# Kernel optimization log

Hardware: AMD Instinct MI355X
Metric: run time of the kernel (lower is better)

## Reference

```python
import jax, jax.numpy as jnp
import numpy as np

LN_EPS = 1e-5

def _ln(x, g, b):
    m = x.mean(-1, keepdims=True)
    v = ((x - m) ** 2).mean(-1, keepdims=True)
    return (x - m) / jnp.sqrt(v + LN_EPS) * g + b

def _mlp(x, W1, b1, g, beta, W2, b2):
    # Linear -> LayerNorm -> ReLU -> Linear
    h = jax.nn.relu(_ln(x @ W1 + b1, g, beta))
    return h @ W2 + b2

def setup_inputs() -> dict:
    key = jax.random.key(0)
    N, E, C_in, C_out, H = 50000, 800000, 64, 64, 64
    ks = jax.random.split(key, 16)
    def rn(k, shape, fan_in):
        return jax.random.normal(k, shape, jnp.float32) * (fan_in ** -0.5)
    return dict(
        x=jax.random.normal(ks[0], (N, C_in), jnp.float32),
        pos=jax.random.normal(ks[1], (N, 3), jnp.float32),
        edge_index=jax.random.randint(ks[2], (2, E), 0, N, jnp.int32),
        W_in=rn(ks[3], (C_in, C_in), C_in), b_in=jnp.zeros((C_in,), jnp.float32),
        W_lin=rn(ks[4], (C_in, C_out), C_in),
        W_src=rn(ks[5], (C_in, C_out), C_in),
        W_dst=rn(ks[6], (C_in, C_out), C_in),
        pos_W1=rn(ks[7], (3, H), 3), pos_b1=jnp.zeros((H,), jnp.float32),
        pos_g=jnp.ones((H,), jnp.float32), pos_beta=jnp.zeros((H,), jnp.float32),
        pos_W2=rn(ks[8], (H, C_out), H), pos_b2=jnp.zeros((C_out,), jnp.float32),
        att_W1=rn(ks[9], (C_out, H), C_out), att_b1=jnp.zeros((H,), jnp.float32),
        att_g=jnp.ones((H,), jnp.float32), att_beta=jnp.zeros((H,), jnp.float32),
        att_W2=rn(ks[10], (H, C_out), H), att_b2=jnp.zeros((C_out,), jnp.float32),
        W_out=rn(ks[11], (C_out, C_out), C_out), b_out=jnp.zeros((C_out,), jnp.float32),
    )

def reference(x, pos, edge_index, W_in, b_in, W_lin, W_src, W_dst,
              pos_W1, pos_b1, pos_g, pos_beta, pos_W2, pos_b2,
              att_W1, att_b1, att_g, att_beta, att_W2, att_b2,
              W_out, b_out):
    N = x.shape[0]
    # lin_in + relu
    x = jax.nn.relu(x @ W_in + b_in)
    # PointTransformerConv with add_self_loops=True (PyG default)
    loops = jnp.arange(N, dtype=edge_index.dtype)
    src = jnp.concatenate([edge_index[0], loops])  # j (neighbors)
    dst = jnp.concatenate([edge_index[1], loops])  # i (centers)
    a_src = x @ W_src           # [N, C_out]
    a_dst = x @ W_dst           # [N, C_out]
    v = x @ W_lin               # [N, C_out]
    # per-edge positional encoding delta = pos_nn(pos_i - pos_j)
    delta = _mlp(pos[dst] - pos[src], pos_W1, pos_b1, pos_g, pos_beta, pos_W2, pos_b2)  # [E, C_out]
    alpha = _mlp(a_dst[dst] - a_src[src] + delta, att_W1, att_b1, att_g, att_beta, att_W2, att_b2)
    # per-destination, per-channel softmax over variable-size neighborhoods
    amax = jax.ops.segment_max(alpha, dst, num_segments=N)
    e = jnp.exp(alpha - amax[dst])
    denom = jax.ops.segment_sum(e, dst, num_segments=N)
    w = e / jnp.clip(denom[dst], 1e-16)
    # weighted scatter-sum of (value_j + delta)
    out = jax.ops.segment_sum(w * (v[src] + delta), dst, num_segments=N)  # [N, C_out]
    # lin_out + relu
    return jax.nn.relu(out @ W_out + b_out)
```

## Files before the change

### kernel.cpp

```cpp
#include <hip/hip_runtime.h>
#include <hip/hip_bf16.h>


typedef __bf16 bf16x8 __attribute__((ext_vector_type(8)));
typedef short  s16x8  __attribute__((ext_vector_type(8)));
typedef float  f32x4  __attribute__((ext_vector_type(4)));

#define SWZ(b) ((b) ^ ((((b) >> 7) & 7) << 4))
#define MAXSEG 16

__device__ __forceinline__ unsigned short f2b(float f) {
  union { __hip_bfloat16 h; unsigned short u; } c;
  c.h = __float2bfloat16(f);
  return c.u;
}
__device__ __forceinline__ unsigned int pack2(float a, float b) {
  return (unsigned int)f2b(a) | ((unsigned int)f2b(b) << 16);
}

__device__ __forceinline__ void stage_wt(const float* __restrict__ W, char* dst, int tid) {
  for (int idx = tid; idx < 2048; idx += 256) {
    int c  = idx >> 5;
    int k2 = (idx & 31) << 1;
    float v0 = W[k2 * 64 + c];
    float v1 = W[(k2 + 1) * 64 + c];
    int byte = c * 128 + k2 * 2;
    *(unsigned int*)(dst + SWZ(byte)) = pack2(v0, v1);
  }
}

__device__ __forceinline__ void gemm64(const char* actb, const char* wb,
                                       int ew, int g, int m, f32x4 acc[4]) {
  #pragma unroll
  for (int kk = 0; kk < 2; kk++) {
    s16x8 af = *(const s16x8*)(actb + SWZ((ew + m) * 128 + g * 16 + kk * 64));
    #pragma unroll
    for (int t = 0; t < 4; t++) {
      s16x8 bf = *(const s16x8*)(wb + SWZ((t * 16 + m) * 128 + g * 16 + kk * 64));
      acc[t] = __builtin_amdgcn_mfma_f32_16x16x32_bf16(
          __builtin_bit_cast(bf16x8, af), __builtin_bit_cast(bf16x8, bf), acc[t], 0, 0, 0);
    }
  }
}

__global__ __launch_bounds__(256, 3) void node_mfma_kernel(
    const float* __restrict__ x,
    const float* __restrict__ W_in, const float* __restrict__ b_in,
    const float* __restrict__ W_lin, const float* __restrict__ W_src, const float* __restrict__ W_dst,
    float* __restrict__ a_src, float* __restrict__ a_dst, float* __restrict__ vv,
    int N)
{
  __shared__ __align__(16) char sWinT[8192], sWsT[8192], sWdT[8192], sWlT[8192], sX[8192];
  __shared__ float sB[64];
  int tid = threadIdx.x;
  stage_wt(W_in,  sWinT, tid);
  stage_wt(W_src, sWsT,  tid);
  stage_wt(W_dst, sWdT,  tid);
  stage_wt(W_lin, sWlT,  tid);
  if (tid < 64) sB[tid] = b_in[tid];

  const int lane = tid & 63, wv = tid >> 6;
  const int g = lane >> 4, m = lane & 15;
  const int ew = wv << 4;
  const int srow = tid >> 2, sc0 = (tid & 3) << 4;
  const int ntile = (N + 63) >> 6;

  for (int tile = blockIdx.x; tile < ntile; tile += gridDim.x) {
    const int rbase = tile << 6;
    __syncthreads();
    {
      int gr = rbase + srow; if (gr >= N) gr = N - 1;
      const float4* src = (const float4*)&x[(size_t)gr * 64 + sc0];
      #pragma unroll
      for (int q = 0; q < 4; q++) {
        float4 f = src[q];
        int byte = srow * 128 + sc0 * 2 + q * 8;
        *(unsigned int*)(sX + SWZ(byte))     = pack2(f.x, f.y);
        *(unsigned int*)(sX + SWZ(byte + 4)) = pack2(f.z, f.w);
      }
    }
    __syncthreads();

    f32x4 a0[4] = {};
    gemm64(sX, sWinT, ew, g, m, a0);
    float x1[4][4];
    #pragma unroll
    for (int t = 0; t < 4; t++)
      #pragma unroll
      for (int r = 0; r < 4; r++) x1[t][r] = fmaxf(a0[t][r] + sB[t * 16 + m], 0.f);
    __syncthreads();
    #pragma unroll
    for (int t = 0; t < 4; t++)
      #pragma unroll
      for (int r = 0; r < 4; r++)
        *(unsigned short*)(sX + SWZ((ew + 4 * g + r) * 128 + (t * 16 + m) * 2)) = f2b(x1[t][r]);
    __syncthreads();

    f32x4 as[4] = {}, ad[4] = {}, al[4] = {};
    gemm64(sX, sWsT, ew, g, m, as);
    gemm64(sX, sWdT, ew, g, m, ad);
    gemm64(sX, sWlT, ew, g, m, al);
    #pragma unroll
    for (int t = 0; t < 4; t++)
      #pragma unroll
      for (int r = 0; r < 4; r++) {
        int gr = rbase + ew + 4 * g + r;
        if (gr < N) {
          size_t o = (size_t)gr * 64 + t * 16 + m;
          a_src[o] = as[t][r]; a_dst[o] = ad[t][r]; vv[o] = al[t][r];
        }
      }
  }
}

__global__ void hist_kernel(const int* __restrict__ ei, int* __restrict__ deg, int E, int Etot) {
  int stride = gridDim.x * blockDim.x;
  for (int e = blockIdx.x * blockDim.x + threadIdx.x; e < Etot; e += stride) {
    int d = (e < E) ? ei[E + e] : (e - E);
    atomicAdd(&deg[d], 1);
  }
}

__global__ __launch_bounds__(256) void scanA_kernel(const int* __restrict__ deg, int* __restrict__ chunkSum, int N) {
  __shared__ int s[256];
  int i = blockIdx.x * 256 + threadIdx.x;
  s[threadIdx.x] = (i < N) ? deg[i] : 0;
  __syncthreads();
  for (int off = 128; off > 0; off >>= 1) {
    if (threadIdx.x < off) s[threadIdx.x] += s[threadIdx.x + off];
    __syncthreads();
  }
  if (threadIdx.x == 0) chunkSum[blockIdx.x] = s[0];
}

__global__ __launch_bounds__(256) void scanB_kernel(const int* __restrict__ chunkSum, int* __restrict__ chunkPre, int nchunk) {
  __shared__ int s[256];
  int t = threadIdx.x;
  int v = (t < nchunk) ? chunkSum[t] : 0;
  s[t] = v; __syncthreads();
  for (int off = 1; off < 256; off <<= 1) {
    int x = (t >= off) ? s[t - off] : 0;
    __syncthreads();
    s[t] += x;
    __syncthreads();
  }
  if (t < nchunk) chunkPre[t] = s[t] - v;
}

__global__ __launch_bounds__(256) void scanC_kernel(const int* __restrict__ deg, const int* __restrict__ chunkPre,
                                                    int* __restrict__ cursor, int N) {
  __shared__ int s[256];
  int t = threadIdx.x;
  int i = blockIdx.x * 256 + t;
  int v = (i < N) ? deg[i] : 0;
  s[t] = v; __syncthreads();
  for (int off = 1; off < 256; off <<= 1) {
    int x = (t >= off) ? s[t - off] : 0;
    __syncthreads();
    s[t] += x;
    __syncthreads();
  }
  if (i < N) cursor[i] = chunkPre[blockIdx.x] + s[t] - v;
}

__global__ void scatter_kernel(const int* __restrict__ ei, int* __restrict__ cursor, int* __restrict__ perm,
                               int E, int Etot) {
  int stride = gridDim.x * blockDim.x;
  for (int e = blockIdx.x * blockDim.x + threadIdx.x; e < Etot; e += stride) {
    int d = (e < E) ? ei[E + e] : (e - E);
    int p = atomicAdd(&cursor[d], 1);
    perm[p] = e;
  }
}

__global__ __launch_bounds__(256, 3) void edge_kernel(
    const float* __restrict__ pos, const int* __restrict__ ei, const int* __restrict__ perm,
    const float* __restrict__ a_src_g, const float* __restrict__ a_dst_g, const float* __restrict__ v_g,
    const float* __restrict__ pos_W1, const float* __restrict__ pos_b1,
    const float* __restrict__ pos_gg, const float* __restrict__ pos_beta,
    const float* __restrict__ pos_W2, const float* __restrict__ pos_b2,
    const float* __restrict__ att_W1, const float* __restrict__ att_b1,
    const float* __restrict__ att_gg, const float* __restrict__ att_beta,
    const float* __restrict__ att_W2, const float* __restrict__ att_b2,
    float* __restrict__ numer, float* __restrict__ denom,
    int E, int Etot)
{
  __shared__ __align__(16) char sW2t[8192], sA1t[8192], sA2t[8192], sAct[8192];
  __shared__ float sAccN[MAXSEG * 64], sAccD[MAXSEG * 64];
  __shared__ float sPW1[192];
  __shared__ float sPB1[64], sPG[64], sPBeta[64], sPB2[64];
  __shared__ float sAB1[64], sAG[64], sABeta[64], sAB2[64];
  __shared__ int   sS[64], sD[64], sSeg[64];
  __shared__ int   sUd[MAXSEG];
  __shared__ int   sNseg;
  __shared__ float sPD[3][64];

  int tid = threadIdx.x;
  stage_wt(pos_W2, sW2t, tid);
  stage_wt(att_W1, sA1t, tid);
  stage_wt(att_W2, sA2t, tid);
  for (int i = tid; i < 192; i += 256) sPW1[i] = pos_W1[i];
  if (tid < 64) {
    sPB1[tid] = pos_b1[tid]; sPG[tid] = pos_gg[tid]; sPBeta[tid] = pos_beta[tid]; sPB2[tid] = pos_b2[tid];
    sAB1[tid] = att_b1[tid]; sAG[tid] = att_gg[tid]; sABeta[tid] = att_beta[tid]; sAB2[tid] = att_b2[tid];
  }

  const int lane = tid & 63, wv = tid >> 6;
  const int g = lane >> 4, m = lane & 15;
  const int ew = wv << 4;
  const int ntile = (Etot + 63) >> 6;

  for (int tile = blockIdx.x; tile < ntile; tile += gridDim.x) {
    const int ebase = tile << 6;
    __syncthreads();

    for (int i = tid; i < MAXSEG * 64; i += 256) { sAccN[i] = 0.f; sAccD[i] = 0.f; }

    if (tid < 64) {
      int slot = ebase + tid;
      int s = 0, d = -1;
      if (slot < Etot) {
        int e = perm[slot];
        if (e < E) { s = ei[e]; d = ei[E + e]; }
        else       { s = e - E; d = s; }
      }
      sS[tid] = s; sD[tid] = d;
      int dm = d < 0 ? 0 : d;
      sPD[0][tid] = pos[dm * 3 + 0] - pos[s * 3 + 0];
      sPD[1][tid] = pos[dm * 3 + 1] - pos[s * 3 + 1];
      sPD[2][tid] = pos[dm * 3 + 2] - pos[s * 3 + 2];
    }
    __syncthreads();

    if (tid < 64) {
      bool valid = sD[tid] >= 0;
      bool flag  = valid && (tid == 0 || sD[tid] != sD[tid - 1]);
      unsigned long long bm = __ballot(flag);
      int cnt = __popcll(bm << (63 - tid));
      sSeg[tid] = valid ? (cnt - 1) : -1;
      if (flag && (cnt - 1) < MAXSEG) sUd[cnt - 1] = sD[tid];
      if (tid == 0) sNseg = __popcll(bm);
    }

    {
      float h[4][4];
      #pragma unroll
      for (int r = 0; r < 4; r++) {
        int er = ew + 4 * g + r;
        float p0 = sPD[0][er], p1 = sPD[1][er], p2 = sPD[2][er];
        #pragma unroll
        for (int t = 0; t < 4; t++) {
          int c = t * 16 + m;
          h[t][r] = fmaf(p0, sPW1[c], fmaf(p1, sPW1[64 + c], fmaf(p2, sPW1[128 + c], sPB1[c])));
        }
      }
      #pragma unroll
      for (int r = 0; r < 4; r++) {
        float s = h[0][r] + h[1][r] + h[2][r] + h[3][r];
        s += __shfl_xor(s, 1); s += __shfl_xor(s, 2); s += __shfl_xor(s, 4); s += __shfl_xor(s, 8);
        float mean = s * (1.f / 64.f);
        float q = 0.f;
        #pragma unroll
        for (int t = 0; t < 4; t++) { float dd = h[t][r] - mean; q = fmaf(dd, dd, q); }
        q += __shfl_xor(q, 1); q += __shfl_xor(q, 2); q += __shfl_xor(q, 4); q += __shfl_xor(q, 8);
        float rs = rsqrtf(q * (1.f / 64.f) + 1e-5f);
        #pragma unroll
        for (int t = 0; t < 4; t++) {
          int c = t * 16 + m;
          float val = fmaxf(fmaf((h[t][r] - mean) * rs, sPG[c], sPBeta[c]), 0.f);
          *(unsigned short*)(sAct + SWZ((ew + 4 * g + r) * 128 + c * 2)) = f2b(val);
        }
      }
    }
    __syncthreads();

    f32x4 dacc[4] = {};
    gemm64(sAct, sW2t, ew, g, m, dacc);
    float del[4][4];
    #pragma unroll
    for (int t = 0; t < 4; t++)
      #pragma unroll
      for (int r = 0; r < 4; r++) del[t][r] = dacc[t][r] + sPB2[t * 16 + m];
    __syncthreads();

    #pragma unroll
    for (int r = 0; r < 4; r++) {
      int er = ew + 4 * g + r;
      int s = sS[er], d = sD[er];
      int dm = d < 0 ? 0 : d;
      #pragma unroll
      for (int t = 0; t < 4; t++) {
        int c = t * 16 + m;
        float a = a_dst_g[(size_t)dm * 64 + c] - a_src_g[(size_t)s * 64 + c] + del[t][r];
        *(unsigned short*)(sAct + SWZ(er * 128 + c * 2)) = f2b(a);
      }
    }
    __syncthreads();

    f32x4 acc2[4] = {};
    gemm64(sAct, sA1t, ew, g, m, acc2);
    float h2[4][4];
    #pragma unroll
    for (int t = 0; t < 4; t++)
      #pragma unroll
      for (int r = 0; r < 4; r++) h2[t][r] = acc2[t][r] + sAB1[t * 16 + m];
    #pragma unroll
    for (int r = 0; r < 4; r++) {
      float s = h2[0][r] + h2[1][r] + h2[2][r] + h2[3][r];
      s += __shfl_xor(s, 1); s += __shfl_xor(s, 2); s += __shfl_xor(s, 4); s += __shfl_xor(s, 8);
      float mean = s * (1.f / 64.f);
      float q = 0.f;
      #pragma unroll
      for (int t = 0; t < 4; t++) { float dd = h2[t][r] - mean; q = fmaf(dd, dd, q); }
      q += __shfl_xor(q, 1); q += __shfl_xor(q, 2); q += __shfl_xor(q, 4); q += __shfl_xor(q, 8);
      float rs = rsqrtf(q * (1.f / 64.f) + 1e-5f);
      #pragma unroll
      for (int t = 0; t < 4; t++) {
        int c = t * 16 + m;
        h2[t][r] = fmaxf(fmaf((h2[t][r] - mean) * rs, sAG[c], sABeta[c]), 0.f);
      }
    }
    __syncthreads();
    #pragma unroll
    for (int t = 0; t < 4; t++)
      #pragma unroll
      for (int r = 0; r < 4; r++)
        *(unsigned short*)(sAct + SWZ((ew + 4 * g + r) * 128 + (t * 16 + m) * 2)) = f2b(h2[t][r]);
    __syncthreads();

    f32x4 acc3[4] = {};
    gemm64(sAct, sA2t, ew, g, m, acc3);

    {
      int curseg = -1, curd = 0;
      float aN[4] = {0.f, 0.f, 0.f, 0.f}, aD[4] = {0.f, 0.f, 0.f, 0.f};
      #pragma unroll
      for (int r = 0; r < 4; r++) {
        int er = ew + 4 * g + r;
        int d = sD[er];
        if (d < 0) continue;
        int seg = sSeg[er];
        if (seg != curseg) {
          if (curseg >= 0) {
            if (curseg < MAXSEG) {
              #pragma unroll
              for (int t = 0; t < 4; t++) {
                atomicAdd(&sAccN[curseg * 64 + t * 16 + m], aN[t]);
                atomicAdd(&sAccD[curseg * 64 + t * 16 + m], aD[t]);
              }
            } else {
              #pragma unroll
              for (int t = 0; t < 4; t++) {
                atomicAdd(&numer[(size_t)curd * 64 + t * 16 + m], aN[t]);
                atomicAdd(&denom[(size_t)curd * 64 + t * 16 + m], aD[t]);
              }
            }
          }
          curseg = seg; curd = d;
          #pragma unroll
          for (int t = 0; t < 4; t++) { aN[t] = 0.f; aD[t] = 0.f; }
        }
        int s = sS[er];
        #pragma unroll
        for (int t = 0; t < 4; t++) {
          int c = t * 16 + m;
          float ee = __expf(acc3[t][r] + sAB2[c]);
          float vvl = v_g[(size_t)s * 64 + c];
          aN[t] = fmaf(ee, vvl + del[t][r], aN[t]);
          aD[t] += ee;
        }
      }
      if (curseg >= 0) {
        if (curseg < MAXSEG) {
          #pragma unroll
          for (int t = 0; t < 4; t++) {
            atomicAdd(&sAccN[curseg * 64 + t * 16 + m], aN[t]);
            atomicAdd(&sAccD[curseg * 64 + t * 16 + m], aD[t]);
          }
        } else {
          #pragma unroll
          for (int t = 0; t < 4; t++) {
            atomicAdd(&numer[(size_t)curd * 64 + t * 16 + m], aN[t]);
            atomicAdd(&denom[(size_t)curd * 64 + t * 16 + m], aD[t]);
          }
        }
      }
    }
    __syncthreads();

    int nseg = sNseg; if (nseg > MAXSEG) nseg = MAXSEG;
    for (int idx = tid; idx < nseg * 64; idx += 256) {
      int seg = idx >> 6, c = idx & 63;
      int d = sUd[seg];
      atomicAdd(&numer[(size_t)d * 64 + c], sAccN[idx]);
      atomicAdd(&denom[(size_t)d * 64 + c], sAccD[idx]);
    }
  }
}

__global__ __launch_bounds__(256) void out_mfma_kernel(
    const float* __restrict__ numer, const float* __restrict__ denom,
    const float* __restrict__ W_out, const float* __restrict__ b_out,
    float* __restrict__ out, int N)
{
  __shared__ __align__(16) char sWoT[8192], sX[8192];
  __shared__ float sB[64];
  int tid = threadIdx.x;
  stage_wt(W_out, sWoT, tid);
  if (tid < 64) sB[tid] = b_out[tid];

  const int lane = tid & 63, wv = tid >> 6;
  const int g = lane >> 4, m = lane & 15;
  const int ew = wv << 4;
  const int srow = tid >> 2, sc0 = (tid & 3) << 4;
  const int ntile = (N + 63) >> 6;

  for (int tile = blockIdx.x; tile < ntile; tile += gridDim.x) {
    const int rbase = tile << 6;
    __syncthreads();
    {
      int gr = rbase + srow; if (gr >= N) gr = N - 1;
      const float4* nsrc = (const float4*)&numer[(size_t)gr * 64 + sc0];
      const float4* dsrc = (const float4*)&denom[(size_t)gr * 64 + sc0];
      #pragma unroll
      for (int q = 0; q < 4; q++) {
        float4 fn = nsrc[q], fd = dsrc[q];
        float m0 = fn.x / fmaxf(fd.x, 1e-16f);
        float m1 = fn.y / fmaxf(fd.y, 1e-16f);
        float m2 = fn.z / fmaxf(fd.z, 1e-16f);
        float m3 = fn.w / fmaxf(fd.w, 1e-16f);
        int byte = srow * 128 + sc0 * 2 + q * 8;
        *(unsigned int*)(sX + SWZ(byte))     = pack2(m0, m1);
        *(unsigned int*)(sX + SWZ(byte + 4)) = pack2(m2, m3);
      }
    }
    __syncthreads();
    f32x4 acc[4] = {};
    gemm64(sX, sWoT, ew, g, m, acc);
    #pragma unroll
    for (int t = 0; t < 4; t++)
      #pragma unroll
      for (int r = 0; r < 4; r++) {
        int gr = rbase + ew + 4 * g + r;
        if (gr < N) out[(size_t)gr * 64 + t * 16 + m] = fmaxf(acc[t][r] + sB[t * 16 + m], 0.f);
      }
  }
}

extern "C" void kernel_launch(void* const* d_in, const int* in_sizes, int n_in,
                              void* d_out, int out_size, void* d_ws, size_t ws_size,
                              hipStream_t stream) {
  (void)n_in; (void)out_size; (void)ws_size;
  const float* x        = (const float*)d_in[0];
  const float* pos      = (const float*)d_in[1];
  const int*   ei       = (const int*)  d_in[2];
  const float* W_in     = (const float*)d_in[3];
  const float* b_in     = (const float*)d_in[4];
  const float* W_lin    = (const float*)d_in[5];
  const float* W_src    = (const float*)d_in[6];
  const float* W_dst    = (const float*)d_in[7];
  const float* pos_W1   = (const float*)d_in[8];
  const float* pos_b1   = (const float*)d_in[9];
  const float* pos_g    = (const float*)d_in[10];
  const float* pos_beta = (const float*)d_in[11];
  const float* pos_W2   = (const float*)d_in[12];
  const float* pos_b2   = (const float*)d_in[13];
  const float* att_W1   = (const float*)d_in[14];
  const float* att_b1   = (const float*)d_in[15];
  const float* att_g    = (const float*)d_in[16];
  const float* att_beta = (const float*)d_in[17];
  const float* att_W2   = (const float*)d_in[18];
  const float* att_b2   = (const float*)d_in[19];
  const float* W_out    = (const float*)d_in[20];
  const float* b_out    = (const float*)d_in[21];

  const int N    = in_sizes[0] / 64;
  const int E    = in_sizes[2] / 2;
  const int Etot = E + N;
  const size_t N64 = (size_t)N * 64;

  float* a_src = (float*)d_ws;
  float* a_dst = a_src + N64;
  float* v     = a_dst + N64;
  float* numer = v + N64;
  float* denom = numer + N64;
  int* deg      = (int*)(denom + N64);
  int* cursor   = deg + N;
  int* chunkSum = cursor + N;
  int* chunkPre = chunkSum + 256;
  int* perm     = chunkPre + 256;

  const int nchunk = (N + 255) / 256;

  hipMemsetAsync(deg, 0, (size_t)N * sizeof(int), stream);
  hipMemsetAsync(numer, 0, 2 * N64 * sizeof(float), stream);

  hist_kernel<<<1024, 256, 0, stream>>>(ei, deg, E, Etot);
  scanA_kernel<<<nchunk, 256, 0, stream>>>(deg, chunkSum, N);
  scanB_kernel<<<1, 256, 0, stream>>>(chunkSum, chunkPre, nchunk);
  scanC_kernel<<<nchunk, 256, 0, stream>>>(deg, chunkPre, cursor, N);
  scatter_kernel<<<1024, 256, 0, stream>>>(ei, cursor, perm, E, Etot);

  const int ntileN = (N + 63) / 64;
  const int nblkN  = ntileN < 768 ? ntileN : 768;
  node_mfma_kernel<<<nblkN, 256, 0, stream>>>(x, W_in, b_in, W_lin, W_src, W_dst,
                                              a_src, a_dst, v, N);

  const int ntile = (Etot + 63) / 64;
  const int nblk  = ntile < 768 ? ntile : 768;
  edge_kernel<<<nblk, 256, 0, stream>>>(pos, ei, perm, a_src, a_dst, v,
      pos_W1, pos_b1, pos_g, pos_beta, pos_W2, pos_b2,
      att_W1, att_b1, att_g, att_beta, att_W2, att_b2,
      numer, denom, E, Etot);

  out_mfma_kernel<<<nblkN, 256, 0, stream>>>(numer, denom, W_out, b_out, (float*)d_out, N);
}
```

Baseline: 470.8 us.

## Make edge kernel wave-independent with per-wave tiles and presorted edge data

Reworks the edge kernel so each wavefront handles its own contiguous 16-edge groups, with a private LDS activation tile and a private segment accumulator. Block-wide __syncthreads are replaced by a waitcnt fence. The scatter kernel now writes sorted src, dst and precomputed pos deltas directly, which removes the perm indirection and the pos gathers from the edge kernel. Gathers of a_src, a_dst and v are issued earlier to hide latency. Padding with memsets and a static group split per wave add some setup cost and may cause load imbalance.

New measurement: 482.2 us. 1.02x slower.

```diff
diff --git a/kernel.cpp b/kernel.cpp
--- a/kernel.cpp
+++ b/kernel.cpp
@@ -7,7 +7,6 @@
 typedef float  f32x4  __attribute__((ext_vector_type(4)));
 
 #define SWZ(b) ((b) ^ ((((b) >> 7) & 7) << 4))
-#define MAXSEG 16
 
 __device__ __forceinline__ unsigned short f2b(float f) {
   union { __hip_bfloat16 h; unsigned short u; } c;
@@ -16,6 +15,10 @@
 }
 __device__ __forceinline__ unsigned int pack2(float a, float b) {
   return (unsigned int)f2b(a) | ((unsigned int)f2b(b) << 16);
+}
+__device__ __forceinline__ void lds_fence() {
+  asm volatile("s_waitcnt lgkmcnt(0)" ::: "memory");
+  __builtin_amdgcn_sched_barrier(0);
 }
 
 __device__ __forceinline__ void stage_wt(const float* __restrict__ W, char* dst, int tid) {
@@ -29,11 +32,11 @@
   }
 }
 
-__device__ __forceinline__ void gemm64(const char* actb, const char* wb,
-                                       int ew, int g, int m, f32x4 acc[4]) {
+__device__ __forceinline__ void gemm16(const char* actb, const char* wb,
+                                       int g, int m, f32x4 acc[4]) {
   #pragma unroll
   for (int kk = 0; kk < 2; kk++) {
-    s16x8 af = *(const s16x8*)(actb + SWZ((ew + m) * 128 + g * 16 + kk * 64));
+    s16x8 af = *(const s16x8*)(actb + SWZ(m * 128 + g * 16 + kk * 64));
     #pragma unroll
     for (int t = 0; t < 4; t++) {
       s16x8 bf = *(const s16x8*)(wb + SWZ((t * 16 + m) * 128 + g * 16 + kk * 64));
@@ -82,7 +85,7 @@
     __syncthreads();
 
     f32x4 a0[4] = {};
-    gemm64(sX, sWinT, ew, g, m, a0);
+    gemm16(sX + ew * 128, sWinT, g, m, a0);
     float x1[4][4];
     #pragma unroll
     for (int t = 0; t < 4; t++)
@@ -97,9 +100,9 @@
     __syncthreads();
 
     f32x4 as[4] = {}, ad[4] = {}, al[4] = {};
-    gemm64(sX, sWsT, ew, g, m, as);
-    gemm64(sX, sWdT, ew, g, m, ad);
-    gemm64(sX, sWlT, ew, g, m, al);
+    gemm16(sX + ew * 128, sWsT, g, m, as);
+    gemm16(sX + ew * 128, sWdT, g, m, ad);
+    gemm16(sX + ew * 128, sWlT, g, m, al);
     #pragma unroll
     for (int t = 0; t < 4; t++)
       #pragma unroll
@@ -163,18 +166,29 @@
   if (i < N) cursor[i] = chunkPre[blockIdx.x] + s[t] - v;
 }
 
-__global__ void scatter_kernel(const int* __restrict__ ei, int* __restrict__ cursor, int* __restrict__ perm,
+__global__ void scatter_kernel(const int* __restrict__ ei, int* __restrict__ cursor,
+                               const float* __restrict__ pos,
+                               int* __restrict__ srcS, int* __restrict__ dstS,
+                               float4* __restrict__ pd4,
                                int E, int Etot) {
   int stride = gridDim.x * blockDim.x;
   for (int e = blockIdx.x * blockDim.x + threadIdx.x; e < Etot; e += stride) {
-    int d = (e < E) ? ei[E + e] : (e - E);
+    int s, d;
+    if (e < E) { s = ei[e]; d = ei[E + e]; }
+    else       { s = e - E; d = s; }
     int p = atomicAdd(&cursor[d], 1);
-    perm[p] = e;
+    srcS[p] = s; dstS[p] = d;
+    float4 q;
+    q.x = pos[d * 3 + 0] - pos[s * 3 + 0];
+    q.y = pos[d * 3 + 1] - pos[s * 3 + 1];
+    q.z = pos[d * 3 + 2] - pos[s * 3 + 2];
+    q.w = 0.f;
+    pd4[p] = q;
   }
 }
 
 __global__ __launch_bounds__(256, 3) void edge_kernel(
-    const float* __restrict__ pos, const int* __restrict__ ei, const int* __restrict__ perm,
+    const int* __restrict__ srcS, const int* __restrict__ dstS, const float4* __restrict__ pd4,
     const float* __restrict__ a_src_g, const float* __restrict__ a_dst_g, const float* __restrict__ v_g,
     const float* __restrict__ pos_W1, const float* __restrict__ pos_b1,
     const float* __restrict__ pos_gg, const float* __restrict__ pos_beta,
@@ -183,17 +197,14 @@
     const float* __restrict__ att_gg, const float* __restrict__ att_beta,
     const float* __restrict__ att_W2, const float* __restrict__ att_b2,
     float* __restrict__ numer, float* __restrict__ denom,
-    int E, int Etot)
+    int G, int gpw)
 {
-  __shared__ __align__(16) char sW2t[8192], sA1t[8192], sA2t[8192], sAct[8192];
-  __shared__ float sAccN[MAXSEG * 64], sAccD[MAXSEG * 64];
+  __shared__ __align__(16) char sW2t[8192], sA1t[8192], sA2t[8192];
+  __shared__ __align__(16) char sAct[4][2048];
+  __shared__ float sAcc[4][4][128];
   __shared__ float sPW1[192];
   __shared__ float sPB1[64], sPG[64], sPBeta[64], sPB2[64];
   __shared__ float sAB1[64], sAG[64], sABeta[64], sAB2[64];
-  __shared__ int   sS[64], sD[64], sSeg[64];
-  __shared__ int   sUd[MAXSEG];
-  __shared__ int   sNseg;
-  __shared__ float sPD[3][64];
 
   int tid = threadIdx.x;
   stage_wt(pos_W2, sW2t, tid);
@@ -204,50 +215,70 @@
     sPB1[tid] = pos_b1[tid]; sPG[tid] = pos_gg[tid]; sPBeta[tid] = pos_beta[tid]; sPB2[tid] = pos_b2[tid];
     sAB1[tid] = att_b1[tid]; sAG[tid] = att_gg[tid]; sABeta[tid] = att_beta[tid]; sAB2[tid] = att_b2[tid];
   }
+  for (int i = tid; i < 4 * 4 * 128; i += 256) ((float*)sAcc)[i] = 0.f;
+  __syncthreads();
 
   const int lane = tid & 63, wv = tid >> 6;
   const int g = lane >> 4, m = lane & 15;
-  const int ew = wv << 4;
-  const int ntile = (Etot + 63) >> 6;
-
-  for (int tile = blockIdx.x; tile < ntile; tile += gridDim.x) {
-    const int ebase = tile << 6;
-    __syncthreads();
-
-    for (int i = tid; i < MAXSEG * 64; i += 256) { sAccN[i] = 0.f; sAccD[i] = 0.f; }
-
-    if (tid < 64) {
-      int slot = ebase + tid;
-      int s = 0, d = -1;
-      if (slot < Etot) {
-        int e = perm[slot];
-        if (e < E) { s = ei[e]; d = ei[E + e]; }
-        else       { s = e - E; d = s; }
-      }
-      sS[tid] = s; sD[tid] = d;
-      int dm = d < 0 ? 0 : d;
-      sPD[0][tid] = pos[dm * 3 + 0] - pos[s * 3 + 0];
-      sPD[1][tid] = pos[dm * 3 + 1] - pos[s * 3 + 1];
-      sPD[2][tid] = pos[dm * 3 + 2] - pos[s * 3 + 2];
-    }
-    __syncthreads();
-
-    if (tid < 64) {
-      bool valid = sD[tid] >= 0;
-      bool flag  = valid && (tid == 0 || sD[tid] != sD[tid - 1]);
-      unsigned long long bm = __ballot(flag);
-      int cnt = __popcll(bm << (63 - tid));
-      sSeg[tid] = valid ? (cnt - 1) : -1;
-      if (flag && (cnt - 1) < MAXSEG) sUd[cnt - 1] = sD[tid];
-      if (tid == 0) sNseg = __popcll(bm);
+  char* myAct = sAct[wv];
+  float (*myAcc)[128] = sAcc[wv];
+
+  const int w  = blockIdx.x * 4 + wv;
+  const int g0 = w * gpw;
+  int g1 = g0 + gpw; if (g1 > G) g1 = G;
+
+  for (int grp = g0; grp < g1; ++grp) {
+    const int ebase = grp << 4;
+
+    float4 pdr[4];
+    #pragma unroll
+    for (int r = 0; r < 4; r++) pdr[r] = pd4[ebase + 4 * g + r];
+    int dall[16];
+    #pragma unroll
+    for (int i = 0; i < 16; i++) dall[i] = dstS[ebase + i];
+    int mys[4];
+    #pragma unroll
+    for (int r = 0; r < 4; r++) mys[r] = srcS[ebase + 4 * g + r];
+
+    int myd[4] = {-1, -1, -1, -1};
+    int sid_my[4] = {0, 0, 0, 0};
+    int fd0 = dall[0], fd1 = -1, fd2 = -1, fd3 = -1;
+    int cur = 0;
+    #pragma unroll
+    for (int i = 0; i < 16; i++) {
+      if (i > 0) {
+        bool b = (dall[i] != dall[i - 1]);
+        cur += b ? 1 : 0;
+        fd1 = (b && cur == 1) ? dall[i] : fd1;
+        fd2 = (b && cur == 2) ? dall[i] : fd2;
+        fd3 = (b && cur == 3) ? dall[i] : fd3;
+      }
+      bool mine = ((i >> 2) == g);
+      const int rr = i & 3;
+      if (rr == 0) { myd[0] = mine ? dall[i] : myd[0]; sid_my[0] = mine ? cur : sid_my[0]; }
+      if (rr == 1) { myd[1] = mine ? dall[i] : myd[1]; sid_my[1] = mine ? cur : sid_my[1]; }
+      if (rr == 2) { myd[2] = mine ? dall[i] : myd[2]; sid_my[2] = mine ? cur : sid_my[2]; }
+      if (rr == 3) { myd[3] = mine ? dall[i] : myd[3]; sid_my[3] = mine ? cur : sid_my[3]; }
+    }
+    const int ns = cur + 1;
+
+    float adst[16], asrc[16];
+    #pragma unroll
+    for (int r = 0; r < 4; r++) {
+      int dm = myd[r] < 0 ? 0 : myd[r];
+      int sm = mys[r];
+      #pragma unroll
+      for (int t = 0; t < 4; t++) {
+        adst[r * 4 + t] = a_dst_g[(size_t)dm * 64 + t * 16 + m];
+        asrc[r * 4 + t] = a_src_g[(size_t)sm * 64 + t * 16 + m];
+      }
     }
 
     {
       float h[4][4];
       #pragma unroll
       for (int r = 0; r < 4; r++) {
-        int er = ew + 4 * g + r;
-        float p0 = sPD[0][er], p1 = sPD[1][er], p2 = sPD[2][er];
+        float p0 = pdr[r].x, p1 = pdr[r].y, p2 = pdr[r].z;
         #pragma unroll
         for (int t = 0; t < 4; t++) {
           int c = t * 16 + m;
@@ -268,37 +299,39 @@
         for (int t = 0; t < 4; t++) {
           int c = t * 16 + m;
           float val = fmaxf(fmaf((h[t][r] - mean) * rs, sPG[c], sPBeta[c]), 0.f);
-          *(unsigned short*)(sAct + SWZ((ew + 4 * g + r) * 128 + c * 2)) = f2b(val);
-        }
-      }
-    }
-    __syncthreads();
+          *(unsigned short*)(myAct + SWZ((4 * g + r) * 128 + c * 2)) = f2b(val);
+        }
+      }
+    }
+    lds_fence();
 
     f32x4 dacc[4] = {};
-    gemm64(sAct, sW2t, ew, g, m, dacc);
+    gemm16(myAct, sW2t, g, m, dacc);
     float del[4][4];
     #pragma unroll
     for (int t = 0; t < 4; t++)
       #pragma unroll
       for (int r = 0; r < 4; r++) del[t][r] = dacc[t][r] + sPB2[t * 16 + m];
-    __syncthreads();
-
-    #pragma unroll
-    for (int r = 0; r < 4; r++) {
-      int er = ew + 4 * g + r;
-      int s = sS[er], d = sD[er];
-      int dm = d < 0 ? 0 : d;
+    lds_fence();
+
+    float vv[16];
+    #pragma unroll
+    for (int r = 0; r < 4; r++)
+      #pragma unroll
+      for (int t = 0; t < 4; t++)
+        vv[r * 4 + t] = v_g[(size_t)mys[r] * 64 + t * 16 + m];
+
+    #pragma unroll
+    for (int r = 0; r < 4; r++)
       #pragma unroll
       for (int t = 0; t < 4; t++) {
-        int c = t * 16 + m;
-        float a = a_dst_g[(size_t)dm * 64 + c] - a_src_g[(size_t)s * 64 + c] + del[t][r];
-        *(unsigned short*)(sAct + SWZ(er * 128 + c * 2)) = f2b(a);
-      }
-    }
-    __syncthreads();
+        float a = adst[r * 4 + t] - asrc[r * 4 + t] + del[t][r];
+        *(unsigned short*)(myAct + SWZ((4 * g + r) * 128 + (t * 16 + m) * 2)) = f2b(a);
+      }
+    lds_fence();
 
     f32x4 acc2[4] = {};
-    gemm64(sAct, sA1t, ew, g, m, acc2);
+    gemm16(myAct, sA1t, g, m, acc2);
     float h2[4][4];
     #pragma unroll
     for (int t = 0; t < 4; t++)
@@ -320,81 +353,87 @@
         h2[t][r] = fmaxf(fmaf((h2[t][r] - mean) * rs, sAG[c], sABeta[c]), 0.f);
       }
     }
-    __syncthreads();
+    lds_fence();
     #pragma unroll
     for (int t = 0; t < 4; t++)
       #pragma unroll
       for (int r = 0; r < 4; r++)
-        *(unsigned short*)(sAct + SWZ((ew + 4 * g + r) * 128 + (t * 16 + m) * 2)) = f2b(h2[t][r]);
-    __syncthreads();
+        *(unsigned short*)(myAct + SWZ((4 * g + r) * 128 + (t * 16 + m) * 2)) = f2b(h2[t][r]);
+    lds_fence();
 
     f32x4 acc3[4] = {};
-    gemm64(sAct, sA2t, ew, g, m, acc3);
+    gemm16(myAct, sA2t, g, m, acc3);
 
     {
-      int curseg = -1, curd = 0;
       float aN[4] = {0.f, 0.f, 0.f, 0.f}, aD[4] = {0.f, 0.f, 0.f, 0.f};
+      int curS = -1, curD = 0;
       #pragma unroll
       for (int r = 0; r < 4; r++) {
-        int er = ew + 4 * g + r;
-        int d = sD[er];
+        int d = myd[r];
         if (d < 0) continue;
-        int seg = sSeg[er];
-        if (seg != curseg) {
-          if (curseg >= 0) {
-            if (curseg < MAXSEG) {
+        int sgid = sid_my[r];
+        if (sgid != curS) {
+          if (curS >= 0) {
+            if (curS < 4) {
               #pragma unroll
               for (int t = 0; t < 4; t++) {
-                atomicAdd(&sAccN[curseg * 64 + t * 16 + m], aN[t]);
-                atomicAdd(&sAccD[curseg * 64 + t * 16 + m], aD[t]);
+                atomicAdd(&myAcc[curS][t * 16 + m], aN[t]);
+                atomicAdd(&myAcc[curS][64 + t * 16 + m], aD[t]);
               }
             } else {
               #pragma unroll
               for (int t = 0; t < 4; t++) {
-                atomicAdd(&numer[(size_t)curd * 64 + t * 16 + m], aN[t]);
-                atomicAdd(&denom[(size_t)curd * 64 + t * 16 + m], aD[t]);
+                atomicAdd(&numer[(size_t)curD * 64 + t * 16 + m], aN[t]);
+                atomicAdd(&denom[(size_t)curD * 64 + t * 16 + m], aD[t]);
               }
             }
           }
-          curseg = seg; curd = d;
+          curS = sgid; curD = d;
           #pragma unroll
           for (int t = 0; t < 4; t++) { aN[t] = 0.f; aD[t] = 0.f; }
         }
-        int s = sS[er];
         #pragma unroll
         for (int t = 0; t < 4; t++) {
-          int c = t * 16 + m;
-          float ee = __expf(acc3[t][r] + sAB2[c]);
-          float vvl = v_g[(size_t)s * 64 + c];
-          aN[t] = fmaf(ee, vvl + del[t][r], aN[t]);
+          float ee = __expf(acc3[t][r] + sAB2[t * 16 + m]);
+          aN[t] = fmaf(ee, vv[r * 4 + t] + del[t][r], aN[t]);
           aD[t] += ee;
         }
       }
-      if (curseg >= 0) {
-        if (curseg < MAXSEG) {
+      if (curS >= 0) {
+        if (curS < 4) {
           #pragma unroll
           for (int t = 0; t < 4; t++) {
-            atomicAdd(&sAccN[curseg * 64 + t * 16 + m], aN[t]);
-            atomicAdd(&sAccD[curseg * 64 + t * 16 + m], aD[t]);
+            atomicAdd(&myAcc[curS][t * 16 + m], aN[t]);
+            atomicAdd(&myAcc[curS][64 + t * 16 + m], aD[t]);
           }
         } else {
           #pragma unroll
           for (int t = 0; t < 4; t++) {
-            atomicAdd(&numer[(size_t)curd * 64 + t * 16 + m], aN[t]);
-            atomicAdd(&denom[(size_t)curd * 64 + t * 16 + m], aD[t]);
+            atomicAdd(&numer[(size_t)curD * 64 + t * 16 + m], aN[t]);
+            atomicAdd(&denom[(size_t)curD * 64 + t * 16 + m], aD[t]);
           }
         }
       }
     }
-    __syncthreads();
-
-    int nseg = sNseg; if (nseg > MAXSEG) nseg = MAXSEG;
-    for (int idx = tid; idx < nseg * 64; idx += 256) {
-      int seg = idx >> 6, c = idx & 63;
-      int d = sUd[seg];
-      atomicAdd(&numer[(size_t)d * 64 + c], sAccN[idx]);
-      atomicAdd(&denom[(size_t)d * 64 + c], sAccD[idx]);
-    }
+    lds_fence();
+
+    {
+      const int nsc = ns < 4 ? ns : 4;
+      const int fdk[1] = {0}; (void)fdk;
+      #pragma unroll
+      for (int k = 0; k < 4; k++) {
+        int dd = (k == 0) ? fd0 : (k == 1) ? fd1 : (k == 2) ? fd2 : fd3;
+        if (k < nsc && dd >= 0) {
+          float nv = myAcc[k][lane];
+          float dv = myAcc[k][64 + lane];
+          atomicAdd(&numer[(size_t)dd * 64 + lane], nv);
+          atomicAdd(&denom[(size_t)dd * 64 + lane], dv);
+          myAcc[k][lane] = 0.f;
+          myAcc[k][64 + lane] = 0.f;
+        }
+      }
+    }
+    lds_fence();
   }
 }
 
@@ -436,7 +475,7 @@
     }
     __syncthreads();
     f32x4 acc[4] = {};
-    gemm64(sX, sWoT, ew, g, m, acc);
+    gemm16(sX + ew * 128, sWoT, g, m, acc);
     #pragma unroll
     for (int t = 0; t < 4; t++)
       #pragma unroll
@@ -477,6 +516,7 @@
   const int N    = in_sizes[0] / 64;
   const int E    = in_sizes[2] / 2;
   const int Etot = E + N;
+  const int Epad = (Etot + 15) & ~15;
   const size_t N64 = (size_t)N * 64;
 
   float* a_src = (float*)d_ws;
@@ -488,30 +528,38 @@
   int* cursor   = deg + N;
   int* chunkSum = cursor + N;
   int* chunkPre = chunkSum + 256;
-  int* perm     = chunkPre + 256;
+  int* srcS     = chunkPre + 256;
+  int* dstS     = srcS + Epad;
+  float4* pd4   = (float4*)(dstS + Epad);
 
   const int nchunk = (N + 255) / 256;
 
   hipMemsetAsync(deg, 0, (size_t)N * sizeof(int), stream);
   hipMemsetAsync(numer, 0, 2 * N64 * sizeof(float), stream);
+  if (Epad > Etot) {
+    hipMemsetAsync(dstS + Etot, 0xFF, (size_t)(Epad - Etot) * sizeof(int), stream);
+    hipMemsetAsync(srcS + Etot, 0, (size_t)(Epad - Etot) * sizeof(int), stream);
+    hipMemsetAsync(pd4 + Etot, 0, (size_t)(Epad - Etot) * sizeof(float4), stream);
+  }
 
   hist_kernel<<<1024, 256, 0, stream>>>(ei, deg, E, Etot);
   scanA_kernel<<<nchunk, 256, 0, stream>>>(deg, chunkSum, N);
   scanB_kernel<<<1, 256, 0, stream>>>(chunkSum, chunkPre, nchunk);
   scanC_kernel<<<nchunk, 256, 0, stream>>>(deg, chunkPre, cursor, N);
-  scatter_kernel<<<1024, 256, 0, stream>>>(ei, cursor, perm, E, Etot);
+  scatter_kernel<<<1024, 256, 0, stream>>>(ei, cursor, pos, srcS, dstS, pd4, E, Etot);
 
   const int ntileN = (N + 63) / 64;
   const int nblkN  = ntileN < 768 ? ntileN : 768;
   node_mfma_kernel<<<nblkN, 256, 0, stream>>>(x, W_in, b_in, W_lin, W_src, W_dst,
                                               a_src, a_dst, v, N);
 
-  const int ntile = (Etot + 63) / 64;
-  const int nblk  = ntile < 768 ? ntile : 768;
-  edge_kernel<<<nblk, 256, 0, stream>>>(pos, ei, perm, a_src, a_dst, v,
+  const int G   = Epad / 16;
+  const int NB  = 768;
+  const int gpw = (G + NB * 4 - 1) / (NB * 4);
+  edge_kernel<<<NB, 256, 0, stream>>>(srcS, dstS, pd4, a_src, a_dst, v,
       pos_W1, pos_b1, pos_g, pos_beta, pos_W2, pos_b2,
       att_W1, att_b1, att_g, att_beta, att_W2, att_b2,
-      numer, denom, E, Etot);
+      numer, denom, G, gpw);
 
   out_mfma_kernel<<<nblkN, 256, 0, stream>>>(numer, denom, W_out, b_out, (float*)d_out, N);
 }
```
